# Kernel optimization log

Measured on AMD Instinct MI355X. Metric: run time of the kernel, lower is better.

The kernel has to match this reference:

```python
import jax, jax.numpy as jnp
import numpy as np

N_NODES = 20000
N_EDGES = 320000
IN_DIM = 512
HID = 256
N_GRAPHS = 256


def setup_inputs() -> dict:
    key = jax.random.key(0)
    ks = jax.random.split(key, 7)
    x = jax.random.normal(ks[0], (N_NODES, IN_DIM), dtype=jnp.float32)
    edge_index = jax.random.randint(ks[1], (2, N_EDGES), 0, N_NODES, dtype=jnp.int64)
    batch = jnp.sort(jax.random.randint(ks[2], (N_NODES,), 0, N_GRAPHS, dtype=jnp.int64))
    W = jax.random.normal(ks[3], (IN_DIM, HID), dtype=jnp.float32) * (1.0 / np.sqrt(IN_DIM))
    b = jax.random.normal(ks[4], (HID,), dtype=jnp.float32) * 0.02
    lin_w = jax.random.normal(ks[5], (HID, 1), dtype=jnp.float32) * (1.0 / np.sqrt(HID))
    lin_b = jax.random.normal(ks[6], (1,), dtype=jnp.float32) * 0.02
    return {"x": x, "edge_index": edge_index, "batch": batch,
            "W": W, "b": b, "lin_w": lin_w, "lin_b": lin_b}


def reference(x, edge_index, batch, W, b, lin_w, lin_b):
    N = x.shape[0]
    # --- GCNConv: add self-loops, symmetric normalization ---
    loop = jnp.arange(N, dtype=edge_index.dtype)
    src = jnp.concatenate([edge_index[0], loop])   # [E+N]
    dst = jnp.concatenate([edge_index[1], loop])   # [E+N]
    deg = jax.ops.segment_sum(jnp.ones_like(dst, dtype=x.dtype), dst, num_segments=N)
    dinv = jnp.where(deg > 0, jax.lax.rsqrt(deg), 0.0)          # [N]
    norm = dinv[src] * dinv[dst]                                 # [E+N]
    h = x @ W                                                    # [N, HID] dense GEMM
    msgs = h[src] * norm[:, None]                                # gather + scale
    agg = jax.ops.segment_sum(msgs, dst, num_segments=N) + b     # scatter-add
    xr = jax.nn.relu(agg)                                        # [N, HID]
    # --- global_mean_pool over graph ids ---
    sums = jax.ops.segment_sum(xr, batch, num_segments=N_GRAPHS)             # [G, HID]
    counts = jax.ops.segment_sum(jnp.ones((N,), dtype=x.dtype), batch, num_segments=N_GRAPHS)
    pooled = sums / jnp.maximum(counts, 1.0)[:, None]
    # --- linear head + sigmoid ---
    out = jax.nn.sigmoid(pooled @ lin_w + lin_b)                 # [G, 1]
    return out.reshape(-1)
```

## Files before the change

### kernel.cpp

```cpp
#include <hip/hip_runtime.h>
#include <hip/hip_bf16.h>
#include <cstdint>

typedef __attribute__((ext_vector_type(8))) _Float16 half8;
typedef __attribute__((ext_vector_type(4))) _Float16 half4;
typedef __attribute__((ext_vector_type(2))) float f32x2;
typedef __attribute__((ext_vector_type(4))) float f32x4;

#define N_NODES 20000
#define N_EDGES 320000
#define IN_DIM 512
#define HID 256
#define N_GRAPHS 256
#define NPB 8
#define ECH 2048

#define PREP_WBLK 16
#define PREP_EBLK (N_EDGES / 256)
#define PREP_BBLK ((N_NODES + 255) / 256)
__global__ __launch_bounds__(256) void prep_kernel(const float* __restrict__ W,
                                                   const int* __restrict__ dst,
                                                   const int* __restrict__ batch,
                                                   _Float16* __restrict__ wt,
                                                   int* __restrict__ ecnt,
                                                   int* __restrict__ counts) {
    int b = blockIdx.x, t = threadIdx.x;
    if (b < PREP_WBLK) {
        __shared__ _Float16 tile[32 * 256];
        int k0 = b * 32;
        const float4* wp = reinterpret_cast<const float4*>(W + (size_t)k0 * HID);
#pragma unroll
        for (int i = 0; i < 8; ++i) {
            float4 v = wp[i * 256 + t];
            int flat = (i * 256 + t) * 4;
            int kk = flat >> 8, n = flat & 255;
            half4 hv;
            hv[0] = (_Float16)v.x; hv[1] = (_Float16)v.y;
            hv[2] = (_Float16)v.z; hv[3] = (_Float16)v.w;
            *reinterpret_cast<half4*>(&tile[kk * 256 + n]) = hv;
        }
        __syncthreads();
        alignas(16) _Float16 vals[32];
#pragma unroll
        for (int kk = 0; kk < 32; ++kk) vals[kk] = tile[kk * 256 + t];
        uint4* op = reinterpret_cast<uint4*>((char*)wt + (size_t)t * 1024 + (size_t)k0 * 2);
        const uint4* vp = reinterpret_cast<const uint4*>(vals);
#pragma unroll
        for (int j = 0; j < 4; ++j) op[j] = vp[j];
    } else if (b < PREP_WBLK + PREP_EBLK) {
        int e = (b - PREP_WBLK) * 256 + t;
        atomicAdd(&ecnt[dst[e]], 1);
    } else {
        int i = (b - PREP_WBLK - PREP_EBLK) * 256 + t;
        if (i < N_NODES) atomicAdd(&counts[batch[i]], 1);
    }
}

__global__ __launch_bounds__(1024) void scan_dinv_kernel(const int* __restrict__ ecnt,
                                                         int* __restrict__ offsets,
                                                         float* __restrict__ dinv) {
    __shared__ int wsum[16];
    int t = threadIdx.x;
    int lane = t & 63, wid = t >> 6;
    const int CHS = 20;
    int base = t * CHS;
    int vals[CHS];
    int s = 0;
    if (t < 1000) {
        const int4* p = reinterpret_cast<const int4*>(ecnt + base);
#pragma unroll
        for (int i = 0; i < 5; ++i) {
            int4 v = p[i];
            vals[4*i+0] = v.x; vals[4*i+1] = v.y; vals[4*i+2] = v.z; vals[4*i+3] = v.w;
        }
#pragma unroll
        for (int i = 0; i < CHS; ++i) s += vals[i];
    }
    int incl = s;
#pragma unroll
    for (int off = 1; off < 64; off <<= 1) {
        int u = __shfl_up(incl, off, 64);
        if (lane >= off) incl += u;
    }
    if (lane == 63) wsum[wid] = incl;
    __syncthreads();
    if (t < 16) {
        int v = wsum[t];
#pragma unroll
        for (int off = 1; off < 16; off <<= 1) {
            int u = __shfl_up(v, off, 16);
            if (t >= off) v += u;
        }
        wsum[t] = v;
    }
    __syncthreads();
    int woff = (wid == 0) ? 0 : wsum[wid - 1];
    if (t < 1000) {
        int run = woff + incl - s;
#pragma unroll
        for (int i = 0; i < CHS; ++i) {
            int idx = base + i;
            offsets[idx] = run;
            dinv[idx] = rsqrtf((float)(vals[i] + 1));
            run += vals[i];
        }
    }
    if (t == 1023) offsets[N_NODES] = wsum[15];
}

#define GEMM_BLOCKS ((N_NODES + 63) / 64)
#define CSR_BLOCKS  ((N_EDGES + 255) / 256)
__global__ __launch_bounds__(256) void gemm_csr_kernel(const float* __restrict__ x,
                                                       const _Float16* __restrict__ wt,
                                                       unsigned char* __restrict__ h8,
                                                       const int* __restrict__ src,
                                                       const int* __restrict__ dst,
                                                       const float* __restrict__ dinv,
                                                       const int* __restrict__ offsets,
                                                       int* __restrict__ cnt2,
                                                       int* __restrict__ csr) {
    __shared__ _Float16 bsl[2 * 256 * 32];
    if (blockIdx.x >= GEMM_BLOCKS) {
        int e = (blockIdx.x - GEMM_BLOCKS) * 256 + threadIdx.x;
        if (e < N_EDGES) {
            int d = dst[e];
            int slot = offsets[d] + atomicAdd(&cnt2[d], 1);
            csr[slot] = src[e];
        }
        return;
    }
    const int K = IN_DIM;
    int t    = threadIdx.x;
    int lane = t & 63;
    int wave = t >> 6;
    int col  = lane & 15;
    int quad = lane >> 4;
    int row0 = blockIdx.x * 64 + wave * 16;

    f32x4 acc[16];
#pragma unroll
    for (int i = 0; i < 16; ++i) acc[i] = (f32x4){0.f, 0.f, 0.f, 0.f};

    int arow = row0 + col;
    if (arow >= N_NODES) arow = N_NODES - 1;
    const float* aptr = x + (size_t)arow * K + quad * 8;
    const uint4* wsrc = reinterpret_cast<const uint4*>(wt + (size_t)t * K);

    float4 pa0 = *reinterpret_cast<const float4*>(aptr);
    float4 pa1 = *reinterpret_cast<const float4*>(aptr + 4);
    uint4 b0 = wsrc[0], b1 = wsrc[1], b2 = wsrc[2], b3 = wsrc[3];

    char* myst = (char*)bsl + t * 64;
    int fsw = (t >> 1) & 3;
    {
        uint4* d = reinterpret_cast<uint4*>(myst);
        d[0 ^ fsw] = b0; d[1 ^ fsw] = b1; d[2 ^ fsw] = b2; d[3 ^ fsw] = b3;
    }
    b0 = wsrc[4]; b1 = wsrc[5]; b2 = wsrc[6]; b3 = wsrc[7];
    asm volatile("s_waitcnt lgkmcnt(0)" ::: "memory");
    __builtin_amdgcn_s_barrier();
    asm volatile("" ::: "memory");

    int p = 0;
    for (int k0 = 0; k0 < K; k0 += 32) {
        half8 a;
        a[0] = (_Float16)pa0.x; a[1] = (_Float16)pa0.y;
        a[2] = (_Float16)pa0.z; a[3] = (_Float16)pa0.w;
        a[4] = (_Float16)pa1.x; a[5] = (_Float16)pa1.y;
        a[6] = (_Float16)pa1.z; a[7] = (_Float16)pa1.w;
        if (k0 + 32 < K) {
            const float* ap = aptr + k0 + 32;
            pa0 = *reinterpret_cast<const float4*>(ap);
            pa1 = *reinterpret_cast<const float4*>(ap + 4);
            uint4* d = reinterpret_cast<uint4*>(myst + ((p ^ 1) << 14));
            d[0 ^ fsw] = b0; d[1 ^ fsw] = b1; d[2 ^ fsw] = b2; d[3 ^ fsw] = b3;
            if (k0 + 64 < K) {
                const uint4* ws = wsrc + ((k0 + 64) >> 3);
                b0 = ws[0]; b1 = ws[1]; b2 = ws[2]; b3 = ws[3];
            }
        }
        const char* rb = (const char*)bsl + (p << 14);
#pragma unroll
        for (int nt = 0; nt < 16; ++nt) {
            int c = nt * 16 + col;
            int fr = (c >> 1) & 3;
            half8 bb = *reinterpret_cast<const half8*>(rb + c * 64 + ((quad ^ fr) << 4));
            acc[nt] = __builtin_amdgcn_mfma_f32_16x16x32_f16(a, bb, acc[nt], 0, 0, 0);
        }
        asm volatile("s_waitcnt lgkmcnt(0)" ::: "memory");
        __builtin_amdgcn_s_barrier();
        asm volatile("" ::: "memory");
        p ^= 1;
    }

    int orow0 = row0 + quad * 4;
    float dv[4];
#pragma unroll
    for (int r = 0; r < 4; ++r) {
        int rr = orow0 + r;
        if (rr >= N_NODES) rr = N_NODES - 1;
        dv[r] = dinv[rr];
    }
#pragma unroll
    for (int nt = 0; nt < 16; ++nt) {
#pragma unroll
        for (int r = 0; r < 4; ++r) {
            int rr = orow0 + r;
            if (rr < N_NODES) {
                float v = acc[nt][r] * dv[r];
                int pk = __builtin_amdgcn_cvt_pk_fp8_f32(v, v, 0, false);
                h8[(size_t)rr * HID + nt * 16 + col] = (unsigned char)(pk & 0xff);
            }
        }
    }
}

__global__ __launch_bounds__(256, 8) void aggregate_kernel(const unsigned char* __restrict__ h8,
                                                           const float* __restrict__ bias,
                                                           const float* __restrict__ dinv,
                                                           const int* __restrict__ offsets,
                                                           const int* __restrict__ csr,
                                                           const int* __restrict__ batch,
                                                           float* __restrict__ sums) {
    __shared__ int s_e[ECH];
    float* pool = reinterpret_cast<float*>(s_e);
    int v0  = blockIdx.x * NPB;
    int t   = threadIdx.x;
    int grp = t >> 6;
    int fl  = t & 63;
    int vg  = v0 + grp * 2;
    const float4 bf = *reinterpret_cast<const float4*>(bias + 4 * fl);

    int off[3];
#pragma unroll
    for (int i = 0; i <= 2; ++i) off[i] = offsets[vg + i];
    int beg0 = offsets[v0], end0 = offsets[v0 + NPB];

    float a0[2], a1[2], a2[2], a3[2], dvv[2];
#pragma unroll
    for (int i = 0; i < 2; ++i) {
        int v = vg + i;
        dvv[i] = dinv[v];
        unsigned int u = *reinterpret_cast<const unsigned int*>(h8 + (size_t)v * HID + 4 * fl);
        f32x2 lo = __builtin_amdgcn_cvt_pk_f32_fp8(u, false);
        f32x2 hi = __builtin_amdgcn_cvt_pk_f32_fp8(u, true);
        a0[i] = lo[0]; a1[i] = lo[1]; a2[i] = hi[0]; a3[i] = hi[1];
    }

    for (int cb = beg0; cb < end0; cb += ECH) {
        int n = min(ECH, end0 - cb);
        for (int tt = t; tt < n; tt += 256) s_e[tt] = csr[cb + tt];
        __syncthreads();
#pragma unroll
        for (int i = 0; i < 2; ++i) {
            int lo_ = off[i] - cb;     if (lo_ < 0) lo_ = 0;
            int hi_ = off[i + 1] - cb; if (hi_ > n) hi_ = n;
            float x0 = a0[i], x1 = a1[i], x2 = a2[i], x3 = a3[i];
            int j = lo_;
            for (; j + 8 <= hi_; j += 8) {
#pragma unroll
                for (int q = 0; q < 8; ++q) {
                    int s = s_e[j + q];
                    unsigned int u = *reinterpret_cast<const unsigned int*>(
                        h8 + (size_t)s * HID + 4 * fl);
                    f32x2 lo = __builtin_amdgcn_cvt_pk_f32_fp8(u, false);
                    f32x2 hi = __builtin_amdgcn_cvt_pk_f32_fp8(u, true);
                    x0 += lo[0]; x1 += lo[1];
                    x2 += hi[0]; x3 += hi[1];
                }
            }
            for (; j < hi_; ++j) {
                int s = s_e[j];
                unsigned int u = *reinterpret_cast<const unsigned int*>(
                    h8 + (size_t)s * HID + 4 * fl);
                f32x2 lo = __builtin_amdgcn_cvt_pk_f32_fp8(u, false);
                f32x2 hi = __builtin_amdgcn_cvt_pk_f32_fp8(u, true);
                x0 += lo[0]; x1 += lo[1];
                x2 += hi[0]; x3 += hi[1];
            }
            a0[i] = x0; a1[i] = x1; a2[i] = x2; a3[i] = x3;
        }
        __syncthreads();
    }

#pragma unroll
    for (int i = 0; i < 2; ++i) {
        f32x4 r;
        r[0] = fmaxf(dvv[i] * a0[i] + bf.x, 0.f);
        r[1] = fmaxf(dvv[i] * a1[i] + bf.y, 0.f);
        r[2] = fmaxf(dvv[i] * a2[i] + bf.z, 0.f);
        r[3] = fmaxf(dvv[i] * a3[i] + bf.w, 0.f);
        *reinterpret_cast<f32x4*>(&pool[(grp * 2 + i) * HID + 4 * fl]) = r;
    }
    __syncthreads();

    float acc = 0.f;
    int cur_g = batch[v0];
#pragma unroll
    for (int i = 0; i < NPB; ++i) {
        float val = pool[i * HID + t];
        int g = batch[v0 + i];
        if (g != cur_g) {
            atomicAdd(&sums[(size_t)cur_g * HID + t], acc);
            acc = 0.f;
            cur_g = g;
        }
        acc += val;
    }
    atomicAdd(&sums[(size_t)cur_g * HID + t], acc);
}

__global__ __launch_bounds__(256) void head_kernel(const float* __restrict__ sums,
                                                   const int* __restrict__ counts,
                                                   const float* __restrict__ lin_w,
                                                   const float* __restrict__ lin_b,
                                                   float* __restrict__ out) {
    int g = blockIdx.x;
    int f = threadIdx.x;
    float c = (float)counts[g];
    if (c < 1.f) c = 1.f;
    float v = (sums[(size_t)g * HID + f] / c) * lin_w[f];
#pragma unroll
    for (int off = 32; off >= 1; off >>= 1) v += __shfl_down(v, off, 64);
    __shared__ float red[4];
    if ((f & 63) == 0) red[f >> 6] = v;
    __syncthreads();
    if (f == 0) {
        float s = red[0] + red[1] + red[2] + red[3] + lin_b[0];
        out[g] = 1.0f / (1.0f + expf(-s));
    }
}

extern "C" void kernel_launch(void* const* d_in, const int* in_sizes, int n_in,
                              void* d_out, int out_size, void* d_ws, size_t ws_size,
                              hipStream_t stream) {
    const float* x     = (const float*)d_in[0];
    const int*   edge  = (const int*)d_in[1];
    const int*   batch = (const int*)d_in[2];
    const float* W     = (const float*)d_in[3];
    const float* b     = (const float*)d_in[4];
    const float* lin_w = (const float*)d_in[5];
    const float* lin_b = (const float*)d_in[6];
    float*       out   = (float*)d_out;

    const int N = N_NODES, E = N_EDGES, G = N_GRAPHS, K = IN_DIM, H = HID;
    const int* src = edge;
    const int* dst = edge + E;

    char* p = (char*)d_ws;
    auto alloc = [&](size_t bytes) {
        char* r = p;
        p += (bytes + 255) & ~(size_t)255;
        return r;
    };
    _Float16*      wt      = (_Float16*)alloc((size_t)H * K * 2);
    unsigned char* h8      = (unsigned char*)alloc((size_t)N * H);
    float*         dinv    = (float*)alloc((size_t)N * 4);
    int*           offsets = (int*)alloc((size_t)(N + 1) * 4);
    int*           csr     = (int*)alloc((size_t)E * 4);
    char* z0 = p;
    int*   ecnt   = (int*)alloc((size_t)N * 4);
    int*   cnt2   = (int*)alloc((size_t)N * 4);
    float* sums   = (float*)alloc((size_t)G * H * 4);
    int*   counts = (int*)alloc((size_t)G * 4);
    size_t zbytes = (size_t)(p - z0);

    hipMemsetAsync(z0, 0, zbytes, stream);

    prep_kernel<<<PREP_WBLK + PREP_EBLK + PREP_BBLK, 256, 0, stream>>>(W, dst, batch,
                                                                       wt, ecnt, counts);
    scan_dinv_kernel<<<1, 1024, 0, stream>>>(ecnt, offsets, dinv);
    gemm_csr_kernel<<<GEMM_BLOCKS + CSR_BLOCKS, 256, 0, stream>>>(x, wt, h8, src, dst,
                                                                  dinv, offsets, cnt2, csr);
    aggregate_kernel<<<N / NPB, 256, 0, stream>>>(h8, b, dinv, offsets, csr, batch, sums);
    head_kernel<<<G, 256, 0, stream>>>(sums, counts, lin_w, lin_b, out);
}
```

Measured before the change: 179.8 us.

## Deepen GEMM prefetch pipeline and split aggregate edges across half-waves with 8-byte gathers

```diff
diff --git a/kernel.cpp b/kernel.cpp
--- a/kernel.cpp
+++ b/kernel.cpp
@@ -146,51 +146,64 @@
     const float* aptr = x + (size_t)arow * K + quad * 8;
     const uint4* wsrc = reinterpret_cast<const uint4*>(wt + (size_t)t * K);
 
-    float4 pa0 = *reinterpret_cast<const float4*>(aptr);
-    float4 pa1 = *reinterpret_cast<const float4*>(aptr + 4);
-    uint4 b0 = wsrc[0], b1 = wsrc[1], b2 = wsrc[2], b3 = wsrc[3];
+    float4 pa0[4], pa1[4];
+#pragma unroll
+    for (int j = 0; j < 4; ++j) {
+        pa0[j] = *reinterpret_cast<const float4*>(aptr + j * 32);
+        pa1[j] = *reinterpret_cast<const float4*>(aptr + j * 32 + 4);
+    }
+    uint4 bw[2][4];
+#pragma unroll
+    for (int j = 0; j < 4; ++j) bw[0][j] = wsrc[j];
 
     char* myst = (char*)bsl + t * 64;
     int fsw = (t >> 1) & 3;
+    int fr  = (col >> 1) & 3;
     {
         uint4* d = reinterpret_cast<uint4*>(myst);
-        d[0 ^ fsw] = b0; d[1 ^ fsw] = b1; d[2 ^ fsw] = b2; d[3 ^ fsw] = b3;
-    }
-    b0 = wsrc[4]; b1 = wsrc[5]; b2 = wsrc[6]; b3 = wsrc[7];
+        d[0 ^ fsw] = bw[0][0]; d[1 ^ fsw] = bw[0][1];
+        d[2 ^ fsw] = bw[0][2]; d[3 ^ fsw] = bw[0][3];
+    }
+#pragma unroll
+    for (int j = 0; j < 4; ++j) bw[1][j] = wsrc[4 + j];
+#pragma unroll
+    for (int j = 0; j < 4; ++j) bw[0][j] = wsrc[8 + j];
     asm volatile("s_waitcnt lgkmcnt(0)" ::: "memory");
     __builtin_amdgcn_s_barrier();
     asm volatile("" ::: "memory");
 
-    int p = 0;
-    for (int k0 = 0; k0 < K; k0 += 32) {
+#pragma unroll
+    for (int s = 0; s < 16; ++s) {
+        const int p = s & 1;
+        float4 q0 = pa0[s & 3], q1 = pa1[s & 3];
         half8 a;
-        a[0] = (_Float16)pa0.x; a[1] = (_Float16)pa0.y;
-        a[2] = (_Float16)pa0.z; a[3] = (_Float16)pa0.w;
-        a[4] = (_Float16)pa1.x; a[5] = (_Float16)pa1.y;
-        a[6] = (_Float16)pa1.z; a[7] = (_Float16)pa1.w;
-        if (k0 + 32 < K) {
-            const float* ap = aptr + k0 + 32;
-            pa0 = *reinterpret_cast<const float4*>(ap);
-            pa1 = *reinterpret_cast<const float4*>(ap + 4);
+        a[0] = (_Float16)q0.x; a[1] = (_Float16)q0.y;
+        a[2] = (_Float16)q0.z; a[3] = (_Float16)q0.w;
+        a[4] = (_Float16)q1.x; a[5] = (_Float16)q1.y;
+        a[6] = (_Float16)q1.z; a[7] = (_Float16)q1.w;
+        if (s + 4 < 16) {
+            pa0[s & 3] = *reinterpret_cast<const float4*>(aptr + (s + 4) * 32);
+            pa1[s & 3] = *reinterpret_cast<const float4*>(aptr + (s + 4) * 32 + 4);
+        }
+        if (s + 1 < 16) {
             uint4* d = reinterpret_cast<uint4*>(myst + ((p ^ 1) << 14));
-            d[0 ^ fsw] = b0; d[1 ^ fsw] = b1; d[2 ^ fsw] = b2; d[3 ^ fsw] = b3;
-            if (k0 + 64 < K) {
-                const uint4* ws = wsrc + ((k0 + 64) >> 3);
-                b0 = ws[0]; b1 = ws[1]; b2 = ws[2]; b3 = ws[3];
+            d[0 ^ fsw] = bw[(s + 1) & 1][0]; d[1 ^ fsw] = bw[(s + 1) & 1][1];
+            d[2 ^ fsw] = bw[(s + 1) & 1][2]; d[3 ^ fsw] = bw[(s + 1) & 1][3];
+            if (s + 3 < 16) {
+#pragma unroll
+                for (int j = 0; j < 4; ++j) bw[(s + 1) & 1][j] = wsrc[(s + 3) * 4 + j];
             }
         }
         const char* rb = (const char*)bsl + (p << 14);
 #pragma unroll
         for (int nt = 0; nt < 16; ++nt) {
-            int c = nt * 16 + col;
-            int fr = (c >> 1) & 3;
-            half8 bb = *reinterpret_cast<const half8*>(rb + c * 64 + ((quad ^ fr) << 4));
+            half8 bb = *reinterpret_cast<const half8*>(
+                rb + (nt * 16 + col) * 64 + ((quad ^ fr) << 4));
             acc[nt] = __builtin_amdgcn_mfma_f32_16x16x32_f16(a, bb, acc[nt], 0, 0, 0);
         }
         asm volatile("s_waitcnt lgkmcnt(0)" ::: "memory");
         __builtin_amdgcn_s_barrier();
         asm volatile("" ::: "memory");
-        p ^= 1;
     }
 
     int orow0 = row0 + quad * 4;
@@ -224,27 +237,34 @@
                                                            float* __restrict__ sums) {
     __shared__ int s_e[ECH];
     float* pool = reinterpret_cast<float*>(s_e);
-    int v0  = blockIdx.x * NPB;
-    int t   = threadIdx.x;
-    int grp = t >> 6;
-    int fl  = t & 63;
-    int vg  = v0 + grp * 2;
-    const float4 bf = *reinterpret_cast<const float4*>(bias + 4 * fl);
+    int v0    = blockIdx.x * NPB;
+    int t     = threadIdx.x;
+    int grp   = t >> 6;
+    int lane  = t & 63;
+    int half_ = lane >> 5;
+    int fl8   = lane & 31;
+    int vg    = v0 + grp * 2;
 
     int off[3];
 #pragma unroll
     for (int i = 0; i <= 2; ++i) off[i] = offsets[vg + i];
     int beg0 = offsets[v0], end0 = offsets[v0 + NPB];
 
-    float a0[2], a1[2], a2[2], a3[2], dvv[2];
+    float acc8[2][8], dvv[2];
+    float selfw = (half_ == 0) ? 1.f : 0.f;
 #pragma unroll
     for (int i = 0; i < 2; ++i) {
         int v = vg + i;
         dvv[i] = dinv[v];
-        unsigned int u = *reinterpret_cast<const unsigned int*>(h8 + (size_t)v * HID + 4 * fl);
-        f32x2 lo = __builtin_amdgcn_cvt_pk_f32_fp8(u, false);
-        f32x2 hi = __builtin_amdgcn_cvt_pk_f32_fp8(u, true);
-        a0[i] = lo[0]; a1[i] = lo[1]; a2[i] = hi[0]; a3[i] = hi[1];
+        uint2 u = *reinterpret_cast<const uint2*>(h8 + (size_t)v * HID + 8 * fl8);
+        f32x2 p0 = __builtin_amdgcn_cvt_pk_f32_fp8(u.x, false);
+        f32x2 p1 = __builtin_amdgcn_cvt_pk_f32_fp8(u.x, true);
+        f32x2 p2 = __builtin_amdgcn_cvt_pk_f32_fp8(u.y, false);
+        f32x2 p3 = __builtin_amdgcn_cvt_pk_f32_fp8(u.y, true);
+        acc8[i][0] = selfw * p0[0]; acc8[i][1] = selfw * p0[1];
+        acc8[i][2] = selfw * p1[0]; acc8[i][3] = selfw * p1[1];
+        acc8[i][4] = selfw * p2[0]; acc8[i][5] = selfw * p2[1];
+        acc8[i][6] = selfw * p3[0]; acc8[i][7] = selfw * p3[1];
     }
 
     for (int cb = beg0; cb < end0; cb += ECH) {
@@ -255,42 +275,66 @@
         for (int i = 0; i < 2; ++i) {
             int lo_ = off[i] - cb;     if (lo_ < 0) lo_ = 0;
             int hi_ = off[i + 1] - cb; if (hi_ > n) hi_ = n;
-            float x0 = a0[i], x1 = a1[i], x2 = a2[i], x3 = a3[i];
+            float x0 = acc8[i][0], x1 = acc8[i][1], x2 = acc8[i][2], x3 = acc8[i][3];
+            float x4 = acc8[i][4], x5 = acc8[i][5], x6 = acc8[i][6], x7 = acc8[i][7];
             int j = lo_;
-            for (; j + 8 <= hi_; j += 8) {
+            for (; j + 16 <= hi_; j += 16) {
 #pragma unroll
                 for (int q = 0; q < 8; ++q) {
-                    int s = s_e[j + q];
-                    unsigned int u = *reinterpret_cast<const unsigned int*>(
-                        h8 + (size_t)s * HID + 4 * fl);
-                    f32x2 lo = __builtin_amdgcn_cvt_pk_f32_fp8(u, false);
-                    f32x2 hi = __builtin_amdgcn_cvt_pk_f32_fp8(u, true);
-                    x0 += lo[0]; x1 += lo[1];
-                    x2 += hi[0]; x3 += hi[1];
+                    int e = s_e[j + 2 * q + half_];
+                    uint2 u = *reinterpret_cast<const uint2*>(
+                        h8 + (size_t)e * HID + 8 * fl8);
+                    f32x2 p0 = __builtin_amdgcn_cvt_pk_f32_fp8(u.x, false);
+                    f32x2 p1 = __builtin_amdgcn_cvt_pk_f32_fp8(u.x, true);
+                    f32x2 p2 = __builtin_amdgcn_cvt_pk_f32_fp8(u.y, false);
+                    f32x2 p3 = __builtin_amdgcn_cvt_pk_f32_fp8(u.y, true);
+                    x0 += p0[0]; x1 += p0[1]; x2 += p1[0]; x3 += p1[1];
+                    x4 += p2[0]; x5 += p2[1]; x6 += p3[0]; x7 += p3[1];
                 }
             }
-            for (; j < hi_; ++j) {
-                int s = s_e[j];
-                unsigned int u = *reinterpret_cast<const unsigned int*>(
-                    h8 + (size_t)s * HID + 4 * fl);
-                f32x2 lo = __builtin_amdgcn_cvt_pk_f32_fp8(u, false);
-                f32x2 hi = __builtin_amdgcn_cvt_pk_f32_fp8(u, true);
-                x0 += lo[0]; x1 += lo[1];
-                x2 += hi[0]; x3 += hi[1];
+            for (; j < hi_; j += 2) {
+                int idx = j + half_;
+                if (idx < hi_) {
+                    int e = s_e[idx];
+                    uint2 u = *reinterpret_cast<const uint2*>(
+                        h8 + (size_t)e * HID + 8 * fl8);
+                    f32x2 p0 = __builtin_amdgcn_cvt_pk_f32_fp8(u.x, false);
+                    f32x2 p1 = __builtin_amdgcn_cvt_pk_f32_fp8(u.x, true);
+                    f32x2 p2 = __builtin_amdgcn_cvt_pk_f32_fp8(u.y, false);
+                    f32x2 p3 = __builtin_amdgcn_cvt_pk_f32_fp8(u.y, true);
+                    x0 += p0[0]; x1 += p0[1]; x2 += p1[0]; x3 += p1[1];
+                    x4 += p2[0]; x5 += p2[1]; x6 += p3[0]; x7 += p3[1];
+                }
             }
-            a0[i] = x0; a1[i] = x1; a2[i] = x2; a3[i] = x3;
+            acc8[i][0] = x0; acc8[i][1] = x1; acc8[i][2] = x2; acc8[i][3] = x3;
+            acc8[i][4] = x4; acc8[i][5] = x5; acc8[i][6] = x6; acc8[i][7] = x7;
         }
         __syncthreads();
     }
 
 #pragma unroll
-    for (int i = 0; i < 2; ++i) {
-        f32x4 r;
-        r[0] = fmaxf(dvv[i] * a0[i] + bf.x, 0.f);
-        r[1] = fmaxf(dvv[i] * a1[i] + bf.y, 0.f);
-        r[2] = fmaxf(dvv[i] * a2[i] + bf.z, 0.f);
-        r[3] = fmaxf(dvv[i] * a3[i] + bf.w, 0.f);
-        *reinterpret_cast<f32x4*>(&pool[(grp * 2 + i) * HID + 4 * fl]) = r;
+    for (int i = 0; i < 2; ++i)
+#pragma unroll
+        for (int k = 0; k < 8; ++k)
+            acc8[i][k] += __shfl_xor(acc8[i][k], 32, 64);
+
+    if (half_ == 0) {
+        const float4 bfa = *reinterpret_cast<const float4*>(bias + 8 * fl8);
+        const float4 bfb = *reinterpret_cast<const float4*>(bias + 8 * fl8 + 4);
+#pragma unroll
+        for (int i = 0; i < 2; ++i) {
+            f32x4 r0, r1;
+            r0[0] = fmaxf(dvv[i] * acc8[i][0] + bfa.x, 0.f);
+            r0[1] = fmaxf(dvv[i] * acc8[i][1] + bfa.y, 0.f);
+            r0[2] = fmaxf(dvv[i] * acc8[i][2] + bfa.z, 0.f);
+            r0[3] = fmaxf(dvv[i] * acc8[i][3] + bfa.w, 0.f);
+            r1[0] = fmaxf(dvv[i] * acc8[i][4] + bfb.x, 0.f);
+            r1[1] = fmaxf(dvv[i] * acc8[i][5] + bfb.y, 0.f);
+            r1[2] = fmaxf(dvv[i] * acc8[i][6] + bfb.z, 0.f);
+            r1[3] = fmaxf(dvv[i] * acc8[i][7] + bfb.w, 0.f);
+            *reinterpret_cast<f32x4*>(&pool[(grp * 2 + i) * HID + 8 * fl8]) = r0;
+            *reinterpret_cast<f32x4*>(&pool[(grp * 2 + i) * HID + 8 * fl8 + 4]) = r1;
+        }
     }
     __syncthreads();
 
```

Result: slower. 234.9 us (+30.7%).

## Interleave CSR scatter with GEMM blocks and privatize degree histograms

Applied to the files above, without the earlier changes.

```diff
diff --git a/kernel.cpp b/kernel.cpp
--- a/kernel.cpp
+++ b/kernel.cpp
@@ -22,9 +22,10 @@
                                                    const int* __restrict__ dst,
                                                    const int* __restrict__ batch,
                                                    _Float16* __restrict__ wt,
-                                                   int* __restrict__ ecnt,
-                                                   int* __restrict__ counts) {
+                                                   int* __restrict__ ecnt8,
+                                                   int* __restrict__ counts8) {
     int b = blockIdx.x, t = threadIdx.x;
+    int slice = b & 7;
     if (b < PREP_WBLK) {
         __shared__ _Float16 tile[32 * 256];
         int k0 = b * 32;
@@ -49,14 +50,14 @@
         for (int j = 0; j < 4; ++j) op[j] = vp[j];
     } else if (b < PREP_WBLK + PREP_EBLK) {
         int e = (b - PREP_WBLK) * 256 + t;
-        atomicAdd(&ecnt[dst[e]], 1);
+        atomicAdd(&ecnt8[slice * N_NODES + dst[e]], 1);
     } else {
         int i = (b - PREP_WBLK - PREP_EBLK) * 256 + t;
-        if (i < N_NODES) atomicAdd(&counts[batch[i]], 1);
-    }
-}
-
-__global__ __launch_bounds__(1024) void scan_dinv_kernel(const int* __restrict__ ecnt,
+        if (i < N_NODES) atomicAdd(&counts8[slice * N_GRAPHS + batch[i]], 1);
+    }
+}
+
+__global__ __launch_bounds__(1024) void scan_dinv_kernel(const int* __restrict__ ecnt8,
                                                          int* __restrict__ offsets,
                                                          float* __restrict__ dinv) {
     __shared__ int wsum[16];
@@ -67,11 +68,15 @@
     int vals[CHS];
     int s = 0;
     if (t < 1000) {
-        const int4* p = reinterpret_cast<const int4*>(ecnt + base);
 #pragma unroll
         for (int i = 0; i < 5; ++i) {
-            int4 v = p[i];
-            vals[4*i+0] = v.x; vals[4*i+1] = v.y; vals[4*i+2] = v.z; vals[4*i+3] = v.w;
+            int4 a = {0, 0, 0, 0};
+#pragma unroll
+            for (int x = 0; x < 8; ++x) {
+                int4 v = *reinterpret_cast<const int4*>(ecnt8 + x * N_NODES + base + 4 * i);
+                a.x += v.x; a.y += v.y; a.z += v.z; a.w += v.w;
+            }
+            vals[4*i+0] = a.x; vals[4*i+1] = a.y; vals[4*i+2] = a.z; vals[4*i+3] = a.w;
         }
 #pragma unroll
         for (int i = 0; i < CHS; ++i) s += vals[i];
@@ -109,7 +114,8 @@
 }
 
 #define GEMM_BLOCKS ((N_NODES + 63) / 64)
-#define CSR_BLOCKS  ((N_EDGES + 255) / 256)
+#define FUSED_GRID  360
+#define SCAT_T      (45 * 256)
 __global__ __launch_bounds__(256) void gemm_csr_kernel(const float* __restrict__ x,
                                                        const _Float16* __restrict__ wt,
                                                        unsigned char* __restrict__ h8,
@@ -120,22 +126,24 @@
                                                        int* __restrict__ cnt2,
                                                        int* __restrict__ csr) {
     __shared__ _Float16 bsl[2 * 256 * 32];
-    if (blockIdx.x >= GEMM_BLOCKS) {
-        int e = (blockIdx.x - GEMM_BLOCKS) * 256 + threadIdx.x;
-        if (e < N_EDGES) {
+    if ((blockIdx.x & 7) == 0) {
+        int tid = (blockIdx.x >> 3) * 256 + threadIdx.x;
+        for (int e = tid; e < N_EDGES; e += SCAT_T) {
             int d = dst[e];
             int slot = offsets[d] + atomicAdd(&cnt2[d], 1);
             csr[slot] = src[e];
         }
         return;
     }
+    int gb = blockIdx.x - (blockIdx.x >> 3) - 1;
+    if (gb >= GEMM_BLOCKS) return;
     const int K = IN_DIM;
     int t    = threadIdx.x;
     int lane = t & 63;
     int wave = t >> 6;
     int col  = lane & 15;
     int quad = lane >> 4;
-    int row0 = blockIdx.x * 64 + wave * 16;
+    int row0 = gb * 64 + wave * 16;
 
     f32x4 acc[16];
 #pragma unroll
@@ -311,13 +319,16 @@
 }
 
 __global__ __launch_bounds__(256) void head_kernel(const float* __restrict__ sums,
-                                                   const int* __restrict__ counts,
+                                                   const int* __restrict__ counts8,
                                                    const float* __restrict__ lin_w,
                                                    const float* __restrict__ lin_b,
                                                    float* __restrict__ out) {
     int g = blockIdx.x;
     int f = threadIdx.x;
-    float c = (float)counts[g];
+    int ci = 0;
+#pragma unroll
+    for (int x = 0; x < 8; ++x) ci += counts8[x * N_GRAPHS + g];
+    float c = (float)ci;
     if (c < 1.f) c = 1.f;
     float v = (sums[(size_t)g * HID + f] / c) * lin_w[f];
 #pragma unroll
@@ -359,19 +370,19 @@
     int*           offsets = (int*)alloc((size_t)(N + 1) * 4);
     int*           csr     = (int*)alloc((size_t)E * 4);
     char* z0 = p;
-    int*   ecnt   = (int*)alloc((size_t)N * 4);
-    int*   cnt2   = (int*)alloc((size_t)N * 4);
-    float* sums   = (float*)alloc((size_t)G * H * 4);
-    int*   counts = (int*)alloc((size_t)G * 4);
+    int*   ecnt8   = (int*)alloc((size_t)8 * N * 4);
+    int*   cnt2    = (int*)alloc((size_t)N * 4);
+    float* sums    = (float*)alloc((size_t)G * H * 4);
+    int*   counts8 = (int*)alloc((size_t)8 * G * 4);
     size_t zbytes = (size_t)(p - z0);
 
     hipMemsetAsync(z0, 0, zbytes, stream);
 
     prep_kernel<<<PREP_WBLK + PREP_EBLK + PREP_BBLK, 256, 0, stream>>>(W, dst, batch,
-                                                                       wt, ecnt, counts);
-    scan_dinv_kernel<<<1, 1024, 0, stream>>>(ecnt, offsets, dinv);
-    gemm_csr_kernel<<<GEMM_BLOCKS + CSR_BLOCKS, 256, 0, stream>>>(x, wt, h8, src, dst,
-                                                                  dinv, offsets, cnt2, csr);
+                                                                       wt, ecnt8, counts8);
+    scan_dinv_kernel<<<1, 1024, 0, stream>>>(ecnt8, offsets, dinv);
+    gemm_csr_kernel<<<FUSED_GRID, 256, 0, stream>>>(x, wt, h8, src, dst,
+                                                    dinv, offsets, cnt2, csr);
     aggregate_kernel<<<N / NPB, 256, 0, stream>>>(h8, b, dinv, offsets, csr, batch, sums);
-    head_kernel<<<G, 256, 0, stream>>>(sums, counts, lin_w, lin_b, out);
-}
+    head_kernel<<<G, 256, 0, stream>>>(sums, counts8, lin_w, lin_b, out);
+}
```

Result: slower. 211.6 us (+17.7%).

## Deepen GEMM K-tile to 64 with two-stage register prefetch and full unroll

Applied to the files above, without the earlier changes.

```diff
diff --git a/kernel.cpp b/kernel.cpp
--- a/kernel.cpp
+++ b/kernel.cpp
@@ -110,16 +110,50 @@
 
 #define GEMM_BLOCKS ((N_NODES + 63) / 64)
 #define CSR_BLOCKS  ((N_EDGES + 255) / 256)
-__global__ __launch_bounds__(256) void gemm_csr_kernel(const float* __restrict__ x,
-                                                       const _Float16* __restrict__ wt,
-                                                       unsigned char* __restrict__ h8,
-                                                       const int* __restrict__ src,
-                                                       const int* __restrict__ dst,
-                                                       const float* __restrict__ dinv,
-                                                       const int* __restrict__ offsets,
-                                                       int* __restrict__ cnt2,
-                                                       int* __restrict__ csr) {
-    __shared__ _Float16 bsl[2 * 256 * 32];
+
+#define LOADA(Sa, Sb, Sc, Sd, k0) do { const float* ap_ = aptr + (k0); \
+    Sa = *reinterpret_cast<const float4*>(ap_);         \
+    Sb = *reinterpret_cast<const float4*>(ap_ + 4);     \
+    Sc = *reinterpret_cast<const float4*>(ap_ + 32);    \
+    Sd = *reinterpret_cast<const float4*>(ap_ + 36); } while (0)
+
+#define PACKA(Sa, Sb, Sc, Sd) do { \
+    a0[0]=(_Float16)Sa.x; a0[1]=(_Float16)Sa.y; a0[2]=(_Float16)Sa.z; a0[3]=(_Float16)Sa.w; \
+    a0[4]=(_Float16)Sb.x; a0[5]=(_Float16)Sb.y; a0[6]=(_Float16)Sb.z; a0[7]=(_Float16)Sb.w; \
+    a1[0]=(_Float16)Sc.x; a1[1]=(_Float16)Sc.y; a1[2]=(_Float16)Sc.z; a1[3]=(_Float16)Sc.w; \
+    a1[4]=(_Float16)Sd.x; a1[5]=(_Float16)Sd.y; a1[6]=(_Float16)Sd.z; a1[7]=(_Float16)Sd.w; } while (0)
+
+#define LOADB(s) do { const uint4* ws_ = wsrc + 8 * (s); \
+    wb0=ws_[0]; wb1=ws_[1]; wb2=ws_[2]; wb3=ws_[3];      \
+    wb4=ws_[4]; wb5=ws_[5]; wb6=ws_[6]; wb7=ws_[7]; } while (0)
+
+#define STAGEB(q) do { uint4* d_ = reinterpret_cast<uint4*>(myst + ((q) << 15)); \
+    d_[0^tsw]=wb0; d_[1^tsw]=wb1; d_[2^tsw]=wb2; d_[3^tsw]=wb3;                  \
+    d_[4^tsw]=wb4; d_[5^tsw]=wb5; d_[6^tsw]=wb6; d_[7^tsw]=wb7; } while (0)
+
+#define KBARRIER() do { asm volatile("s_waitcnt lgkmcnt(0)" ::: "memory"); \
+    __builtin_amdgcn_s_barrier(); asm volatile("" ::: "memory"); } while (0)
+
+#define MFMASTEP(q) do { const char* rb_ = (const char*)bsl + ((q) << 15); \
+    _Pragma("unroll")                                                      \
+    for (int nt = 0; nt < 16; ++nt) {                                      \
+        int c_ = nt * 16 + col; int cs_ = c_ & 7;                          \
+        half8 bb0_ = *reinterpret_cast<const half8*>(rb_ + c_ * 128 + ((quad ^ cs_) << 4));       \
+        acc[nt] = __builtin_amdgcn_mfma_f32_16x16x32_f16(a0, bb0_, acc[nt], 0, 0, 0);             \
+        half8 bb1_ = *reinterpret_cast<const half8*>(rb_ + c_ * 128 + (((4 + quad) ^ cs_) << 4)); \
+        acc[nt] = __builtin_amdgcn_mfma_f32_16x16x32_f16(a1, bb1_, acc[nt], 0, 0, 0);             \
+    } } while (0)
+
+__global__ __launch_bounds__(256, 2) void gemm_csr_kernel(const float* __restrict__ x,
+                                                          const _Float16* __restrict__ wt,
+                                                          unsigned char* __restrict__ h8,
+                                                          const int* __restrict__ src,
+                                                          const int* __restrict__ dst,
+                                                          const float* __restrict__ dinv,
+                                                          const int* __restrict__ offsets,
+                                                          int* __restrict__ cnt2,
+                                                          int* __restrict__ csr) {
+    __shared__ _Float16 bsl[2 * 256 * 64];
     if (blockIdx.x >= GEMM_BLOCKS) {
         int e = (blockIdx.x - GEMM_BLOCKS) * 256 + threadIdx.x;
         if (e < N_EDGES) {
@@ -146,51 +180,34 @@
     const float* aptr = x + (size_t)arow * K + quad * 8;
     const uint4* wsrc = reinterpret_cast<const uint4*>(wt + (size_t)t * K);
 
-    float4 pa0 = *reinterpret_cast<const float4*>(aptr);
-    float4 pa1 = *reinterpret_cast<const float4*>(aptr + 4);
-    uint4 b0 = wsrc[0], b1 = wsrc[1], b2 = wsrc[2], b3 = wsrc[3];
-
-    char* myst = (char*)bsl + t * 64;
-    int fsw = (t >> 1) & 3;
-    {
-        uint4* d = reinterpret_cast<uint4*>(myst);
-        d[0 ^ fsw] = b0; d[1 ^ fsw] = b1; d[2 ^ fsw] = b2; d[3 ^ fsw] = b3;
-    }
-    b0 = wsrc[4]; b1 = wsrc[5]; b2 = wsrc[6]; b3 = wsrc[7];
-    asm volatile("s_waitcnt lgkmcnt(0)" ::: "memory");
-    __builtin_amdgcn_s_barrier();
-    asm volatile("" ::: "memory");
-
-    int p = 0;
-    for (int k0 = 0; k0 < K; k0 += 32) {
-        half8 a;
-        a[0] = (_Float16)pa0.x; a[1] = (_Float16)pa0.y;
-        a[2] = (_Float16)pa0.z; a[3] = (_Float16)pa0.w;
-        a[4] = (_Float16)pa1.x; a[5] = (_Float16)pa1.y;
-        a[6] = (_Float16)pa1.z; a[7] = (_Float16)pa1.w;
-        if (k0 + 32 < K) {
-            const float* ap = aptr + k0 + 32;
-            pa0 = *reinterpret_cast<const float4*>(ap);
-            pa1 = *reinterpret_cast<const float4*>(ap + 4);
-            uint4* d = reinterpret_cast<uint4*>(myst + ((p ^ 1) << 14));
-            d[0 ^ fsw] = b0; d[1 ^ fsw] = b1; d[2 ^ fsw] = b2; d[3 ^ fsw] = b3;
-            if (k0 + 64 < K) {
-                const uint4* ws = wsrc + ((k0 + 64) >> 3);
-                b0 = ws[0]; b1 = ws[1]; b2 = ws[2]; b3 = ws[3];
-            }
-        }
-        const char* rb = (const char*)bsl + (p << 14);
-#pragma unroll
-        for (int nt = 0; nt < 16; ++nt) {
-            int c = nt * 16 + col;
-            int fr = (c >> 1) & 3;
-            half8 bb = *reinterpret_cast<const half8*>(rb + c * 64 + ((quad ^ fr) << 4));
-            acc[nt] = __builtin_amdgcn_mfma_f32_16x16x32_f16(a, bb, acc[nt], 0, 0, 0);
-        }
-        asm volatile("s_waitcnt lgkmcnt(0)" ::: "memory");
-        __builtin_amdgcn_s_barrier();
-        asm volatile("" ::: "memory");
-        p ^= 1;
+    char* myst = (char*)bsl + t * 128;
+    int tsw = t & 7;
+
+    float4 sA0, sA1, sA2, sA3;
+    float4 sB0, sB1, sB2, sB3;
+    uint4  wb0, wb1, wb2, wb3, wb4, wb5, wb6, wb7;
+    half8  a0, a1;
+
+    LOADB(0);
+    LOADA(sA0, sA1, sA2, sA3, 0);
+    LOADA(sB0, sB1, sB2, sB3, 64);
+    STAGEB(0);
+    LOADB(1);
+    KBARRIER();
+
+#pragma unroll
+    for (int it = 0; it < 4; ++it) {
+        PACKA(sA0, sA1, sA2, sA3);
+        if (it < 3) LOADA(sA0, sA1, sA2, sA3, (2 * it + 2) * 64);
+        STAGEB(1);
+        if (it < 3) LOADB(2 * it + 2);
+        MFMASTEP(0);
+        KBARRIER();
+        PACKA(sB0, sB1, sB2, sB3);
+        if (it < 3) LOADA(sB0, sB1, sB2, sB3, (2 * it + 3) * 64);
+        if (it < 3) { STAGEB(0); LOADB(2 * it + 3); }
+        MFMASTEP(1);
+        KBARRIER();
     }
 
     int orow0 = row0 + quad * 4;
```

After: 181.6 us. No clear change (+1.0%).
